# Performance work log

Measured on AMD Instinct MI355X. Metric: run time of the kernel, lower is better.

The kernel has to match this reference:

```python
import jax, jax.numpy as jnp
import numpy as np

DIM = 512
NUM_HEADS = 16
RANK = 4
HEAD_DIM = DIM // NUM_HEADS
SCALE = HEAD_DIM ** -0.5
B_, N, NW = 2048, 49, 64


def setup_inputs() -> dict:
    key = jax.random.key(0)
    ks = jax.random.split(key, 9)
    x = jax.random.normal(ks[0], (B_, N, DIM), dtype=jnp.float32)
    mask = jax.random.normal(ks[1], (NW, N, N), dtype=jnp.float32)
    # qkv base linear (torch Linear stores weight [out,in])
    W_qkv = jax.random.normal(ks[2], (3 * DIM, DIM), dtype=jnp.float32) * (DIM ** -0.5)
    b_qkv = jax.random.normal(ks[3], (3 * DIM,), dtype=jnp.float32) * 0.02
    # LoRA down [rank, dim], up [3*dim, rank] (zero-init in module; use small random for non-trivial math)
    A_down = jax.random.normal(ks[4], (RANK, DIM), dtype=jnp.float32) * 0.02
    B_up = jax.random.normal(ks[5], (3 * DIM, RANK), dtype=jnp.float32) * 0.02
    W_proj = jax.random.normal(ks[6], (DIM, DIM), dtype=jnp.float32) * (DIM ** -0.5)
    b_proj = jax.random.normal(ks[7], (DIM,), dtype=jnp.float32) * 0.02
    return {"x": x, "mask": mask, "W_qkv": W_qkv, "b_qkv": b_qkv,
            "A_down": A_down, "B_up": B_up, "W_proj": W_proj, "b_proj": b_proj}


def reference(x, mask, W_qkv, b_qkv, A_down, B_up, W_proj, b_proj):
    Bw, n, C = x.shape
    H, hd = NUM_HEADS, HEAD_DIM
    # LoRA-augmented QKV projection: base linear + up(down(x))
    qkv = x @ W_qkv.T + b_qkv + (x @ A_down.T) @ B_up.T          # [B_, N, 3C]
    qkv = qkv.reshape(Bw, n, 3, H, hd)
    q = qkv[:, :, 0].transpose(0, 2, 1, 3)                        # [B_, H, N, hd]
    k = qkv[:, :, 1].transpose(0, 2, 1, 3)
    v = qkv[:, :, 2].transpose(0, 2, 1, 3)
    attn = jnp.einsum('bhnd,bhmd->bhnm', q, k) * SCALE            # [B_, H, N, N]
    nW = mask.shape[0]
    attn = attn.reshape(Bw // nW, nW, H, n, n) + mask[None, :, None]
    attn = attn.reshape(Bw, H, n, n)
    attn = jax.nn.softmax(attn, axis=-1)
    out = jnp.einsum('bhnm,bhmd->bhnd', attn, v)                  # [B_, H, N, hd]
    out = out.transpose(0, 2, 1, 3).reshape(Bw, n, C)
    return out @ W_proj.T + b_proj
```

## Files before the change

kernel.cpp:

```cpp
#include <hip/hip_runtime.h>
#include <stdint.h>

typedef __attribute__((ext_vector_type(4))) float f32x4;
typedef __attribute__((ext_vector_type(8))) __bf16 bf16x8;
typedef __attribute__((ext_vector_type(4))) unsigned int u32x4;
typedef __attribute__((ext_vector_type(4))) unsigned short u16x4;

#define TOK 49
#define NHEAD 16
#define HDIM 32
#define CDIM 512
#define NB 2048
#define MTOT (NB * TOK)
#define ATT_SCALE 0.17677669529663687f

__device__ __forceinline__ unsigned short f2bf(float f) {
  uint32_t u = __builtin_bit_cast(uint32_t, f);
  u += 0x7FFFu + ((u >> 16) & 1u);
  return (unsigned short)(u >> 16);
}

__device__ __forceinline__ void gl_lds16(const void* g, const void* lds) {
  __builtin_amdgcn_global_load_lds(
      (__attribute__((address_space(1))) void*)(uintptr_t)g,
      (__attribute__((address_space(3))) void*)(uint32_t)(uintptr_t)lds,
      16, 0, 0);
}

__device__ __forceinline__ f32x4 mfma16(bf16x8 a, bf16x8 b, f32x4 c) {
  return __builtin_amdgcn_mfma_f32_16x16x32_bf16(a, b, c, 0, 0, 0);
}

__global__ __launch_bounds__(256) void k_prep_weff(
    const float* __restrict__ Wqkv, const float* __restrict__ Bup,
    const float* __restrict__ Adown, unsigned short* __restrict__ weff) {
  int idx = blockIdx.x * 256 + threadIdx.x;
  if (idx >= 3 * CDIM * CDIM) return;
  int o = idx >> 9, i = idx & 511;
  float v = Wqkv[idx];
#pragma unroll
  for (int r = 0; r < 4; r++) v += Bup[o * 4 + r] * Adown[r * 512 + i];
  weff[idx] = f2bf(v);
}

__global__ __launch_bounds__(256) void k_conv4(
    const float* __restrict__ src, unsigned short* __restrict__ dst, int n4) {
  for (int i = blockIdx.x * blockDim.x + threadIdx.x; i < n4;
       i += gridDim.x * blockDim.x) {
    f32x4 v = *(const f32x4*)(src + (size_t)i * 4);
    u16x4 o;
    o[0] = f2bf(v[0]); o[1] = f2bf(v[1]); o[2] = f2bf(v[2]); o[3] = f2bf(v[3]);
    *(u16x4*)(dst + (size_t)i * 4) = o;
  }
}

template <int NT, bool SPLIT, bool AF32>
__global__ __launch_bounds__(512, 1) void k_gemm256(
    const void* __restrict__ Ain, const unsigned short* __restrict__ Bw,
    const float* __restrict__ bias,
    unsigned short* __restrict__ qo, unsigned short* __restrict__ ko,
    unsigned short* __restrict__ vo, float* __restrict__ fo) {
  __shared__ __attribute__((aligned(16))) unsigned short smem[65536];
  const unsigned short* Ab = (const unsigned short*)Ain;
  const float* Af = (const float*)Ain;
  const int t = threadIdx.x;
  const int l = t & 63;
  const int l15 = l & 15, lq = l >> 4;
  const int w = t >> 6;
  const int wr = w >> 2, wc = w & 3;
  const int bid = blockIdx.x;
  const int lb = (bid & 7) * ((int)gridDim.x >> 3) + (bid >> 3);
  const int mt = lb / NT, nt = lb % NT;
  const size_t m0 = (size_t)mt * 256;
  const int n0 = nt * 256;

  auto stageA = [&](int kt, int bb) {
    unsigned short* dst = smem + bb * 16384;
#pragma unroll
    for (int q = 0; q < 4; ++q) {
      const int li = q * 512 + t;
      const int row = li >> 3, sl = li & 7;
      gl_lds16(Ab + (m0 + row) * CDIM + kt * 64 + ((sl ^ (row & 7)) << 3),
               &dst[li * 8]);
    }
  };
  auto stageB = [&](int kt, int bb) {
    unsigned short* dst = smem + 32768 + bb * 16384;
#pragma unroll
    for (int q = 0; q < 4; ++q) {
      const int li = q * 512 + t;
      const int row = li >> 3, sl = li & 7;
      gl_lds16(Bw + (size_t)(n0 + row) * CDIM + kt * 64 + ((sl ^ (row & 7)) << 3),
               &dst[li * 8]);
    }
  };

  f32x4 ar[4];
  auto issueAh = [&](int kt, int h) {
#pragma unroll
    for (int q = 0; q < 2; ++q) {
      const int li = (h * 2 + q) * 512 + t;
      const int row = li >> 3, sl = li & 7;
      const float* p =
          Af + (m0 + row) * CDIM + kt * 64 + ((sl ^ (row & 7)) << 3);
      ar[q * 2] = *(const f32x4*)p;
      ar[q * 2 + 1] = *(const f32x4*)(p + 4);
    }
  };
  auto writeAh = [&](int bb, int h) {
    unsigned short* dst = smem + bb * 16384;
#pragma unroll
    for (int q = 0; q < 2; ++q) {
      const int li = (h * 2 + q) * 512 + t;
      u32x4 wv;
      wv[0] = (uint32_t)f2bf(ar[q * 2][0]) | ((uint32_t)f2bf(ar[q * 2][1]) << 16);
      wv[1] = (uint32_t)f2bf(ar[q * 2][2]) | ((uint32_t)f2bf(ar[q * 2][3]) << 16);
      wv[2] = (uint32_t)f2bf(ar[q * 2 + 1][0]) |
              ((uint32_t)f2bf(ar[q * 2 + 1][1]) << 16);
      wv[3] = (uint32_t)f2bf(ar[q * 2 + 1][2]) |
              ((uint32_t)f2bf(ar[q * 2 + 1][3]) << 16);
      *(u32x4*)&dst[li * 8] = wv;
    }
  };

  f32x4 acc[8][4] = {};
  if constexpr (AF32) {
    issueAh(0, 0);
    stageB(0, 0);
    writeAh(0, 0);
    issueAh(0, 1);
    writeAh(0, 1);
    asm volatile("s_waitcnt lgkmcnt(0)" ::: "memory");
  } else {
    stageA(0, 0);
    stageB(0, 0);
  }

  for (int kt = 0; kt < 8; ++kt) {
    const int cur = kt & 1, nb = cur ^ 1;
    if (kt < 7) {
      if constexpr (AF32) issueAh(kt + 1, 0);
      else stageA(kt + 1, nb);
      stageB(kt + 1, nb);
      asm volatile("s_waitcnt vmcnt(8)" ::: "memory");
    } else {
      asm volatile("s_waitcnt vmcnt(0)" ::: "memory");
    }
    __builtin_amdgcn_s_barrier();
    asm volatile("" ::: "memory");
    const unsigned short* bufA = smem + cur * 16384;
    const unsigned short* bufB = smem + 32768 + cur * 16384;

    bf16x8 bfr[4][2];
#pragma unroll
    for (int c = 0; c < 4; ++c) {
      const int r = wc * 64 + c * 16 + l15;
#pragma unroll
      for (int h = 0; h < 2; ++h)
        bfr[c][h] = __builtin_bit_cast(
            bf16x8,
            *(const u32x4*)&bufB[r * 64 + (((lq + h * 4) ^ (r & 7)) << 3)]);
    }

#pragma unroll
    for (int p = 0; p < 4; ++p) {
      bf16x8 af[2][2];
#pragma unroll
      for (int rr = 0; rr < 2; ++rr) {
        const int r = wr * 128 + (p * 2 + rr) * 16 + l15;
#pragma unroll
        for (int h = 0; h < 2; ++h)
          af[rr][h] = __builtin_bit_cast(
              bf16x8,
              *(const u32x4*)&bufA[r * 64 + (((lq + h * 4) ^ (r & 7)) << 3)]);
      }
      __builtin_amdgcn_s_setprio(1);
#pragma unroll
      for (int rr = 0; rr < 2; ++rr) {
#pragma unroll
        for (int c = 0; c < 4; ++c) {
          acc[p * 2 + rr][c] = mfma16(af[rr][0], bfr[c][0], acc[p * 2 + rr][c]);
          acc[p * 2 + rr][c] = mfma16(af[rr][1], bfr[c][1], acc[p * 2 + rr][c]);
        }
      }
      __builtin_amdgcn_s_setprio(0);
      if constexpr (AF32) {
        if (p == 1 && kt < 7) {
          writeAh(nb, 0);
          issueAh(kt + 1, 1);
        }
        if (p == 3 && kt < 7) writeAh(nb, 1);
      }
    }
    if constexpr (AF32)
      asm volatile("s_waitcnt lgkmcnt(0)" ::: "memory");
    asm volatile("" ::: "memory");
    __builtin_amdgcn_s_barrier();
  }

  __syncthreads();
  if constexpr (SPLIT) {
    unsigned short* ep = smem + w * 8192;
#pragma unroll
    for (int J = 0; J < 4; ++J) {
      const int colb = n0 + wc * 64 + J * 16 + l15;
      const float bv = bias[colb];
      const int sl0 = J * 2 + (l15 >> 3);
#pragma unroll
      for (int I = 0; I < 8; ++I) {
#pragma unroll
        for (int r = 0; r < 4; ++r) {
          const int row = I * 16 + lq * 4 + r;
          ep[row * 64 + ((sl0 ^ (row & 7)) << 3) + (l15 & 7)] =
              f2bf(acc[I][J][r] + bv);
        }
      }
    }
    __syncthreads();
#pragma unroll
    for (int rnd = 0; rnd < 16; ++rnd) {
      const int sub = rnd * 16 + (l >> 2);
      const int mloc = sub >> 1, hd2 = sub & 1;
      const int colh = n0 + wc * 64 + hd2 * 32;
      const int which = colh >> 9;
      const int hh = (colh >> 5) & 15;
      unsigned short* dst = which == 0 ? qo : (which == 1 ? ko : vo);
      const uint32_t mg = (uint32_t)(m0 + wr * 128 + mloc);
      const uint32_t bw_ = mg / 49u;
      const uint32_t nn = mg - bw_ * 49u;
      const int sl = hd2 * 4 + (l & 3);
      u32x4 v = *(const u32x4*)&ep[mloc * 64 + ((sl ^ (mloc & 7)) << 3)];
      *(u32x4*)&dst[((size_t)(bw_ * 16u + hh) * 49u + nn) * 32u + (l & 3) * 8] =
          v;
    }
  } else {
    float* ep32 = (float*)smem + w * 4096;
#pragma unroll
    for (int ch = 0; ch < 2; ++ch) {
#pragma unroll
      for (int J = 0; J < 4; ++J) {
        const int colb = n0 + wc * 64 + J * 16 + l15;
        const float bv = bias[colb];
        const int sl0 = J * 4 + (l15 >> 2);
#pragma unroll
        for (int Ii = 0; Ii < 4; ++Ii) {
#pragma unroll
          for (int r = 0; r < 4; ++r) {
            const int row = Ii * 16 + lq * 4 + r;
            ep32[row * 64 + ((sl0 ^ (row & 7)) << 2) + (l15 & 3)] =
                acc[ch * 4 + Ii][J][r] + bv;
          }
        }
      }
      __syncthreads();
#pragma unroll
      for (int rnd = 0; rnd < 16; ++rnd) {
        const int row = rnd * 4 + (l >> 4);
        const int sl = l & 15;
        f32x4 v = *(const f32x4*)&ep32[row * 64 + ((sl ^ (row & 7)) << 2)];
        const size_t mg = m0 + wr * 128 + ch * 64 + row;
        *(f32x4*)&fo[mg * CDIM + n0 + wc * 64 + (l & 15) * 4] = v;
      }
      __syncthreads();
    }
  }
}

__global__ __launch_bounds__(256) void k_attn(
    const unsigned short* __restrict__ qb, const unsigned short* __restrict__ kb,
    const unsigned short* __restrict__ vb, const float* __restrict__ mask,
    unsigned short* __restrict__ ao) {
  __shared__ __attribute__((aligned(16))) unsigned short sP[4][64 * 64];
  __shared__ __attribute__((aligned(16))) unsigned short sV[4][32 * 64];
  const int t = threadIdx.x;
  const int l = t & 63, w = t >> 6;
  const int l15 = l & 15, lq = l >> 4;
  const int pair = blockIdx.x * 4 + w;
  const int b = pair >> 4, h = pair & 15;
  const size_t base = (size_t)pair * (TOK * HDIM);
  unsigned short* P = sP[w];
  unsigned short* Vt = sV[w];

  bf16x8 qf[4], kf[4];
#pragma unroll
  for (int i = 0; i < 4; i++)
    qf[i] = __builtin_bit_cast(
        bf16x8, *(const u32x4*)(qb + base + (size_t)(i * 16 + l15) * 32 + lq * 8));
#pragma unroll
  for (int i = 0; i < 4; i++)
    kf[i] = __builtin_bit_cast(
        bf16x8, *(const u32x4*)(kb + base + (size_t)(i * 16 + l15) * 32 + lq * 8));
  u32x4 vr[4];
#pragma unroll
  for (int j = 0; j < 4; j++)
    vr[j] = *(const u32x4*)(vb + base + (size_t)l * 32 + j * 8);

  f32x4 s[4][4];
  __builtin_amdgcn_s_setprio(1);
#pragma unroll
  for (int i = 0; i < 4; i++) {
#pragma unroll
    for (int j = 0; j < 4; j++) s[i][j] = mfma16(qf[i], kf[j], (f32x4)0.0f);
  }
  __builtin_amdgcn_s_setprio(0);

  const bool vok = (l < TOK);
  const int tsl = ((l >> 3) & 7);
  const int tlo = l & 7;
#pragma unroll
  for (int j = 0; j < 4; j++) {
#pragma unroll
    for (int c = 0; c < 4; c++) {
      uint32_t u = vr[j][c];
      int d0 = j * 8 + c * 2;
      Vt[(d0 + 0) * 64 + ((tsl ^ ((d0 + 0) & 7)) << 3) + tlo] =
          vok ? (unsigned short)(u & 0xFFFFu) : (unsigned short)0;
      Vt[(d0 + 1) * 64 + ((tsl ^ ((d0 + 1) & 7)) << 3) + tlo] =
          vok ? (unsigned short)(u >> 16) : (unsigned short)0;
    }
  }

  const float* mrow = mask + (size_t)(b & 63) * (TOK * TOK);
#pragma unroll
  for (int i = 0; i < 4; i++) {
#pragma unroll
    for (int r = 0; r < 4; r++) {
      int row = i * 16 + lq * 4 + r;
#pragma unroll
      for (int j = 0; j < 4; j++) {
        int col = j * 16 + l15;
        float xv = s[i][j][r] * ATT_SCALE;
        if (col < TOK) {
          if (row < TOK) xv += mrow[row * TOK + col];
        } else {
          xv = -1e30f;
        }
        s[i][j][r] = xv;
      }
    }
  }

  float rinv[4][4];
#pragma unroll
  for (int i = 0; i < 4; i++) {
#pragma unroll
    for (int r = 0; r < 4; r++) {
      float m = fmaxf(fmaxf(s[i][0][r], s[i][1][r]), fmaxf(s[i][2][r], s[i][3][r]));
      m = fmaxf(m, __shfl_xor(m, 1));
      m = fmaxf(m, __shfl_xor(m, 2));
      m = fmaxf(m, __shfl_xor(m, 4));
      m = fmaxf(m, __shfl_xor(m, 8));
      float sum = 0.f;
      int row = i * 16 + lq * 4 + r;
#pragma unroll
      for (int j = 0; j < 4; j++) {
        float p = __expf(s[i][j][r] - m);
        sum += p;
        P[row * 64 + (((j * 2 + (l15 >> 3)) ^ (row & 7)) << 3) + (l15 & 7)] =
            f2bf(p);
      }
      sum += __shfl_xor(sum, 1);
      sum += __shfl_xor(sum, 2);
      sum += __shfl_xor(sum, 4);
      sum += __shfl_xor(sum, 8);
      rinv[i][r] = 1.0f / sum;
    }
  }

  asm volatile("s_waitcnt lgkmcnt(0)" ::: "memory");
  __builtin_amdgcn_sched_barrier(0);

  f32x4 o[4][2] = {};
#pragma unroll
  for (int ks = 0; ks < 2; ks++) {
    bf16x8 pa[4], vf[2];
#pragma unroll
    for (int i = 0; i < 4; i++)
      pa[i] = __builtin_bit_cast(
          bf16x8,
          *(const u32x4*)&P[(i * 16 + l15) * 64 + (((lq + ks * 4) ^ (l15 & 7)) << 3)]);
#pragma unroll
    for (int j = 0; j < 2; j++)
      vf[j] = __builtin_bit_cast(
          bf16x8,
          *(const u32x4*)&Vt[(j * 16 + l15) * 64 + (((lq + ks * 4) ^ (l15 & 7)) << 3)]);
    __builtin_amdgcn_s_setprio(1);
#pragma unroll
    for (int i = 0; i < 4; i++) {
#pragma unroll
      for (int j = 0; j < 2; j++) o[i][j] = mfma16(pa[i], vf[j], o[i][j]);
    }
    __builtin_amdgcn_s_setprio(0);
  }

#pragma unroll
  for (int i = 0; i < 4; i++) {
#pragma unroll
    for (int r = 0; r < 4; r++) {
      int row = i * 16 + lq * 4 + r;
      if (row < TOK) {
        float inv = rinv[i][r];
        size_t obase = ((size_t)b * TOK + row) * CDIM + h * HDIM;
#pragma unroll
        for (int j = 0; j < 2; j++)
          ao[obase + j * 16 + l15] = f2bf(o[i][j][r] * inv);
      }
    }
  }
}

extern "C" void kernel_launch(void* const* d_in, const int* in_sizes, int n_in,
                              void* d_out, int out_size, void* d_ws,
                              size_t ws_size, hipStream_t stream) {
  const float* x = (const float*)d_in[0];
  const float* mask = (const float*)d_in[1];
  const float* Wqkv = (const float*)d_in[2];
  const float* bqkv = (const float*)d_in[3];
  const float* Adown = (const float*)d_in[4];
  const float* Bup = (const float*)d_in[5];
  const float* Wproj = (const float*)d_in[6];
  const float* bproj = (const float*)d_in[7];
  float* out = (float*)d_out;
  char* ws = (char*)d_ws;

  size_t off = 0;
  auto alloc = [&](size_t bytes) {
    size_t o = off;
    off += (bytes + 255) & ~(size_t)255;
    return o;
  };
  const size_t qkv_elems = (size_t)NB * NHEAD * TOK * HDIM;
  unsigned short* weff = (unsigned short*)(ws + alloc((size_t)3 * CDIM * CDIM * 2));
  unsigned short* wpb = (unsigned short*)(ws + alloc((size_t)CDIM * CDIM * 2));
  unsigned short* qb = (unsigned short*)(ws + alloc(qkv_elems * 2 + 4096));
  unsigned short* kb = (unsigned short*)(ws + alloc(qkv_elems * 2 + 4096));
  unsigned short* vb = (unsigned short*)(ws + alloc(qkv_elems * 2 + 4096));
  unsigned short* ao = (unsigned short*)(ws + alloc((size_t)MTOT * CDIM * 2));

  k_prep_weff<<<(3 * CDIM * CDIM + 255) / 256, 256, 0, stream>>>(Wqkv, Bup,
                                                                 Adown, weff);
  k_conv4<<<256, 256, 0, stream>>>(Wproj, wpb, CDIM * CDIM / 4);
  k_gemm256<6, true, true><<<(MTOT / 256) * 6, 512, 0, stream>>>(
      x, weff, bqkv, qb, kb, vb, nullptr);
  k_attn<<<NB * NHEAD / 4, 256, 0, stream>>>(qb, kb, vb, mask, ao);
  k_gemm256<2, false, false><<<(MTOT / 256) * 2, 512, 0, stream>>>(
      ao, wpb, bproj, nullptr, nullptr, nullptr, out);
}
```

Measured before the change: 583.4 us.

## Pre-convert x to bf16 and use a smaller-tile GEMM for output projection

The QKV GEMM no longer reads fp32 x and converts it in registers inside the K loop. A separate conversion kernel writes a bf16 copy of x first, and the GEMM stages A through direct global-to-LDS loads. The output projection moves from the 256x256 one-block-per-CU GEMM to a new 128x128 kernel with 256 threads and up to three blocks per CU, which gives more blocks for the N=512 problem. The cost is an extra full pass over x (read fp32, write bf16), and the bf16 buffer aliases the attention output workspace.

```diff
diff --git a/kernel.cpp b/kernel.cpp
--- a/kernel.cpp
+++ b/kernel.cpp
@@ -54,15 +54,12 @@
   }
 }
 
-template <int NT, bool SPLIT, bool AF32>
-__global__ __launch_bounds__(512, 1) void k_gemm256(
-    const void* __restrict__ Ain, const unsigned short* __restrict__ Bw,
+__global__ __launch_bounds__(512, 1) void k_gemm256qkv(
+    const unsigned short* __restrict__ A, const unsigned short* __restrict__ Bw,
     const float* __restrict__ bias,
     unsigned short* __restrict__ qo, unsigned short* __restrict__ ko,
-    unsigned short* __restrict__ vo, float* __restrict__ fo) {
+    unsigned short* __restrict__ vo) {
   __shared__ __attribute__((aligned(16))) unsigned short smem[65536];
-  const unsigned short* Ab = (const unsigned short*)Ain;
-  const float* Af = (const float*)Ain;
   const int t = threadIdx.x;
   const int l = t & 63;
   const int l15 = l & 15, lq = l >> 4;
@@ -70,7 +67,7 @@
   const int wr = w >> 2, wc = w & 3;
   const int bid = blockIdx.x;
   const int lb = (bid & 7) * ((int)gridDim.x >> 3) + (bid >> 3);
-  const int mt = lb / NT, nt = lb % NT;
+  const int mt = lb / 6, nt = lb % 6;
   const size_t m0 = (size_t)mt * 256;
   const int n0 = nt * 256;
 
@@ -80,7 +77,7 @@
     for (int q = 0; q < 4; ++q) {
       const int li = q * 512 + t;
       const int row = li >> 3, sl = li & 7;
-      gl_lds16(Ab + (m0 + row) * CDIM + kt * 64 + ((sl ^ (row & 7)) << 3),
+      gl_lds16(A + (m0 + row) * CDIM + kt * 64 + ((sl ^ (row & 7)) << 3),
                &dst[li * 8]);
     }
   };
@@ -95,52 +92,13 @@
     }
   };
 
-  f32x4 ar[4];
-  auto issueAh = [&](int kt, int h) {
-#pragma unroll
-    for (int q = 0; q < 2; ++q) {
-      const int li = (h * 2 + q) * 512 + t;
-      const int row = li >> 3, sl = li & 7;
-      const float* p =
-          Af + (m0 + row) * CDIM + kt * 64 + ((sl ^ (row & 7)) << 3);
-      ar[q * 2] = *(const f32x4*)p;
-      ar[q * 2 + 1] = *(const f32x4*)(p + 4);
-    }
-  };
-  auto writeAh = [&](int bb, int h) {
-    unsigned short* dst = smem + bb * 16384;
-#pragma unroll
-    for (int q = 0; q < 2; ++q) {
-      const int li = (h * 2 + q) * 512 + t;
-      u32x4 wv;
-      wv[0] = (uint32_t)f2bf(ar[q * 2][0]) | ((uint32_t)f2bf(ar[q * 2][1]) << 16);
-      wv[1] = (uint32_t)f2bf(ar[q * 2][2]) | ((uint32_t)f2bf(ar[q * 2][3]) << 16);
-      wv[2] = (uint32_t)f2bf(ar[q * 2 + 1][0]) |
-              ((uint32_t)f2bf(ar[q * 2 + 1][1]) << 16);
-      wv[3] = (uint32_t)f2bf(ar[q * 2 + 1][2]) |
-              ((uint32_t)f2bf(ar[q * 2 + 1][3]) << 16);
-      *(u32x4*)&dst[li * 8] = wv;
-    }
-  };
-
   f32x4 acc[8][4] = {};
-  if constexpr (AF32) {
-    issueAh(0, 0);
-    stageB(0, 0);
-    writeAh(0, 0);
-    issueAh(0, 1);
-    writeAh(0, 1);
-    asm volatile("s_waitcnt lgkmcnt(0)" ::: "memory");
-  } else {
-    stageA(0, 0);
-    stageB(0, 0);
-  }
-
+  stageA(0, 0);
+  stageB(0, 0);
   for (int kt = 0; kt < 8; ++kt) {
     const int cur = kt & 1, nb = cur ^ 1;
     if (kt < 7) {
-      if constexpr (AF32) issueAh(kt + 1, 0);
-      else stageA(kt + 1, nb);
+      stageA(kt + 1, nb);
       stageB(kt + 1, nb);
       asm volatile("s_waitcnt vmcnt(8)" ::: "memory");
     } else {
@@ -184,85 +142,153 @@
         }
       }
       __builtin_amdgcn_s_setprio(0);
-      if constexpr (AF32) {
-        if (p == 1 && kt < 7) {
-          writeAh(nb, 0);
-          issueAh(kt + 1, 1);
-        }
-        if (p == 3 && kt < 7) writeAh(nb, 1);
-      }
-    }
-    if constexpr (AF32)
-      asm volatile("s_waitcnt lgkmcnt(0)" ::: "memory");
+    }
     asm volatile("" ::: "memory");
     __builtin_amdgcn_s_barrier();
   }
 
   __syncthreads();
-  if constexpr (SPLIT) {
-    unsigned short* ep = smem + w * 8192;
+  unsigned short* ep = smem + w * 8192;
+#pragma unroll
+  for (int J = 0; J < 4; ++J) {
+    const int colb = n0 + wc * 64 + J * 16 + l15;
+    const float bv = bias[colb];
+    const int sl0 = J * 2 + (l15 >> 3);
+#pragma unroll
+    for (int I = 0; I < 8; ++I) {
+#pragma unroll
+      for (int r = 0; r < 4; ++r) {
+        const int row = I * 16 + lq * 4 + r;
+        ep[row * 64 + ((sl0 ^ (row & 7)) << 3) + (l15 & 7)] =
+            f2bf(acc[I][J][r] + bv);
+      }
+    }
+  }
+  __syncthreads();
+#pragma unroll
+  for (int rnd = 0; rnd < 16; ++rnd) {
+    const int sub = rnd * 16 + (l >> 2);
+    const int mloc = sub >> 1, hd2 = sub & 1;
+    const int colh = n0 + wc * 64 + hd2 * 32;
+    const int which = colh >> 9;
+    const int hh = (colh >> 5) & 15;
+    unsigned short* dst = which == 0 ? qo : (which == 1 ? ko : vo);
+    const uint32_t mg = (uint32_t)(m0 + wr * 128 + mloc);
+    const uint32_t bw_ = mg / 49u;
+    const uint32_t nn = mg - bw_ * 49u;
+    const int sl = hd2 * 4 + (l & 3);
+    u32x4 v = *(const u32x4*)&ep[mloc * 64 + ((sl ^ (mloc & 7)) << 3)];
+    *(u32x4*)&dst[((size_t)(bw_ * 16u + hh) * 49u + nn) * 32u + (l & 3) * 8] = v;
+  }
+}
+
+__global__ __launch_bounds__(256, 3) void k_gemm128(
+    const unsigned short* __restrict__ A, const unsigned short* __restrict__ Bw,
+    const float* __restrict__ bias, float* __restrict__ fo) {
+  __shared__ __attribute__((aligned(16))) unsigned short smem[16384];
+  const int t = threadIdx.x;
+  const int l = t & 63;
+  const int l15 = l & 15, lq = l >> 4;
+  const int w = t >> 6;
+  const int wr = w >> 1, wc = w & 1;
+  const int bid = blockIdx.x;
+  const int lb = (bid & 7) * ((int)gridDim.x >> 3) + (bid >> 3);
+  const int mt = lb / 4, nt = lb % 4;
+  const size_t m0 = (size_t)mt * 128;
+  const int n0 = nt * 128;
+
+  auto stageA = [&](int kt, int bb) {
+    unsigned short* dst = smem + bb * 4096;
+#pragma unroll
+    for (int q = 0; q < 2; ++q) {
+      const int li = q * 256 + t;
+      const int row = li >> 2, sl = li & 3;
+      gl_lds16(A + (m0 + row) * CDIM + kt * 32 + ((sl ^ ((row >> 1) & 3)) << 3),
+               &dst[li * 8]);
+    }
+  };
+  auto stageB = [&](int kt, int bb) {
+    unsigned short* dst = smem + 8192 + bb * 4096;
+#pragma unroll
+    for (int q = 0; q < 2; ++q) {
+      const int li = q * 256 + t;
+      const int row = li >> 2, sl = li & 3;
+      gl_lds16(Bw + (size_t)(n0 + row) * CDIM + kt * 32 +
+                   ((sl ^ ((row >> 1) & 3)) << 3),
+               &dst[li * 8]);
+    }
+  };
+
+  f32x4 acc[4][4] = {};
+  stageA(0, 0);
+  stageB(0, 0);
+  for (int kt = 0; kt < 16; ++kt) {
+    const int cur = kt & 1, nb = cur ^ 1;
+    if (kt < 15) {
+      stageA(kt + 1, nb);
+      stageB(kt + 1, nb);
+      asm volatile("s_waitcnt vmcnt(4)" ::: "memory");
+    } else {
+      asm volatile("s_waitcnt vmcnt(0)" ::: "memory");
+    }
+    __builtin_amdgcn_s_barrier();
+    asm volatile("" ::: "memory");
+    const unsigned short* bufA = smem + cur * 4096;
+    const unsigned short* bufB = smem + 8192 + cur * 4096;
+    bf16x8 af[4], bfv[4];
+#pragma unroll
+    for (int f = 0; f < 4; ++f) {
+      const int r = wr * 64 + f * 16 + l15;
+      af[f] = __builtin_bit_cast(
+          bf16x8, *(const u32x4*)&bufA[r * 32 + ((lq ^ ((r >> 1) & 3)) << 3)]);
+    }
+#pragma unroll
+    for (int c = 0; c < 4; ++c) {
+      const int r = wc * 64 + c * 16 + l15;
+      bfv[c] = __builtin_bit_cast(
+          bf16x8, *(const u32x4*)&bufB[r * 32 + ((lq ^ ((r >> 1) & 3)) << 3)]);
+    }
+    __builtin_amdgcn_s_setprio(1);
+#pragma unroll
+    for (int f = 0; f < 4; ++f) {
+#pragma unroll
+      for (int c = 0; c < 4; ++c) acc[f][c] = mfma16(af[f], bfv[c], acc[f][c]);
+    }
+    __builtin_amdgcn_s_setprio(0);
+    asm volatile("" ::: "memory");
+    __builtin_amdgcn_s_barrier();
+  }
+
+  __syncthreads();
+  float* ep32 = (float*)smem + w * 2048;
+#pragma unroll
+  for (int ch = 0; ch < 2; ++ch) {
 #pragma unroll
     for (int J = 0; J < 4; ++J) {
       const int colb = n0 + wc * 64 + J * 16 + l15;
       const float bv = bias[colb];
-      const int sl0 = J * 2 + (l15 >> 3);
-#pragma unroll
-      for (int I = 0; I < 8; ++I) {
+      const int sl0 = J * 4 + (l15 >> 2);
+#pragma unroll
+      for (int Ii = 0; Ii < 2; ++Ii) {
 #pragma unroll
         for (int r = 0; r < 4; ++r) {
-          const int row = I * 16 + lq * 4 + r;
-          ep[row * 64 + ((sl0 ^ (row & 7)) << 3) + (l15 & 7)] =
-              f2bf(acc[I][J][r] + bv);
+          const int row = Ii * 16 + lq * 4 + r;
+          ep32[row * 64 + ((sl0 ^ (row & 7)) << 2) + (l15 & 3)] =
+              acc[ch * 2 + Ii][J][r] + bv;
         }
       }
     }
-    __syncthreads();
-#pragma unroll
-    for (int rnd = 0; rnd < 16; ++rnd) {
-      const int sub = rnd * 16 + (l >> 2);
-      const int mloc = sub >> 1, hd2 = sub & 1;
-      const int colh = n0 + wc * 64 + hd2 * 32;
-      const int which = colh >> 9;
-      const int hh = (colh >> 5) & 15;
-      unsigned short* dst = which == 0 ? qo : (which == 1 ? ko : vo);
-      const uint32_t mg = (uint32_t)(m0 + wr * 128 + mloc);
-      const uint32_t bw_ = mg / 49u;
-      const uint32_t nn = mg - bw_ * 49u;
-      const int sl = hd2 * 4 + (l & 3);
-      u32x4 v = *(const u32x4*)&ep[mloc * 64 + ((sl ^ (mloc & 7)) << 3)];
-      *(u32x4*)&dst[((size_t)(bw_ * 16u + hh) * 49u + nn) * 32u + (l & 3) * 8] =
-          v;
-    }
-  } else {
-    float* ep32 = (float*)smem + w * 4096;
-#pragma unroll
-    for (int ch = 0; ch < 2; ++ch) {
-#pragma unroll
-      for (int J = 0; J < 4; ++J) {
-        const int colb = n0 + wc * 64 + J * 16 + l15;
-        const float bv = bias[colb];
-        const int sl0 = J * 4 + (l15 >> 2);
-#pragma unroll
-        for (int Ii = 0; Ii < 4; ++Ii) {
-#pragma unroll
-          for (int r = 0; r < 4; ++r) {
-            const int row = Ii * 16 + lq * 4 + r;
-            ep32[row * 64 + ((sl0 ^ (row & 7)) << 2) + (l15 & 3)] =
-                acc[ch * 4 + Ii][J][r] + bv;
-          }
-        }
-      }
-      __syncthreads();
-#pragma unroll
-      for (int rnd = 0; rnd < 16; ++rnd) {
-        const int row = rnd * 4 + (l >> 4);
-        const int sl = l & 15;
-        f32x4 v = *(const f32x4*)&ep32[row * 64 + ((sl ^ (row & 7)) << 2)];
-        const size_t mg = m0 + wr * 128 + ch * 64 + row;
-        *(f32x4*)&fo[mg * CDIM + n0 + wc * 64 + (l & 15) * 4] = v;
-      }
-      __syncthreads();
-    }
+    asm volatile("s_waitcnt lgkmcnt(0)" ::: "memory");
+#pragma unroll
+    for (int rnd = 0; rnd < 8; ++rnd) {
+      const int row = rnd * 4 + (l >> 4);
+      const int sl = l & 15;
+      f32x4 v = *(const f32x4*)&ep32[row * 64 + ((sl ^ (row & 7)) << 2)];
+      const size_t mg = m0 + wr * 64 + ch * 32 + row;
+      *(f32x4*)&fo[mg * CDIM + n0 + wc * 64 + (l & 15) * 4] = v;
+    }
+    asm volatile("s_waitcnt lgkmcnt(0)" ::: "memory");
+    asm volatile("" ::: "memory");
   }
 }
 
@@ -435,14 +461,14 @@
   unsigned short* qb = (unsigned short*)(ws + alloc(qkv_elems * 2 + 4096));
   unsigned short* kb = (unsigned short*)(ws + alloc(qkv_elems * 2 + 4096));
   unsigned short* vb = (unsigned short*)(ws + alloc(qkv_elems * 2 + 4096));
-  unsigned short* ao = (unsigned short*)(ws + alloc((size_t)MTOT * CDIM * 2));
+  unsigned short* xb = (unsigned short*)(ws + alloc((size_t)MTOT * CDIM * 2));
+  unsigned short* ao = xb;
 
   k_prep_weff<<<(3 * CDIM * CDIM + 255) / 256, 256, 0, stream>>>(Wqkv, Bup,
                                                                  Adown, weff);
   k_conv4<<<256, 256, 0, stream>>>(Wproj, wpb, CDIM * CDIM / 4);
-  k_gemm256<6, true, true><<<(MTOT / 256) * 6, 512, 0, stream>>>(
-      x, weff, bqkv, qb, kb, vb, nullptr);
+  k_conv4<<<2048, 256, 0, stream>>>(x, xb, MTOT * CDIM / 4);
+  k_gemm256qkv<<<(MTOT / 256) * 6, 512, 0, stream>>>(xb, weff, bqkv, qb, kb, vb);
   k_attn<<<NB * NHEAD / 4, 256, 0, stream>>>(qb, kb, vb, mask, ao);
-  k_gemm256<2, false, false><<<(MTOT / 256) * 2, 512, 0, stream>>>(
-      ao, wpb, bproj, nullptr, nullptr, nullptr, out);
-}
+  k_gemm128<<<(MTOT / 128) * 4, 256, 0, stream>>>(ao, wpb, bproj, out);
+}
```

New measurement: 561.4 us. 3.8% less time.
